# Kernel optimization log

Measured on AMD Instinct MI355X. Metric: run time of the kernel, lower is better.

Reference implementation:

```python
import jax, jax.numpy as jnp
import numpy as np
import math

NUM_HEADS = 16
MAX_BIAS = 8.0

def _alibi_slopes(n_heads):
    def slopes(n):
        start = 2.0 ** (-2 ** (-(math.log2(n) - 3)))
        return [start * start ** i for i in range(n)]
    if math.log2(n_heads).is_integer():
        s = slopes(n_heads)
    else:
        p = 2 ** math.floor(math.log2(n_heads))
        s = slopes(p) + slopes(2 * p)[0::2][: n_heads - p]
    return jnp.asarray(np.array(s, dtype=np.float32))

def setup_inputs() -> dict:
    key = jax.random.key(0)
    ks = jax.random.split(key, 5)
    B, S, C = 2, 2048, 1024
    return {
        "x": jax.random.normal(ks[0], (B, S, C), jnp.float32),
        "in_proj_weight": jax.random.normal(ks[1], (3 * C, C), jnp.float32) * (C ** -0.5),
        "in_proj_bias": jax.random.normal(ks[2], (3 * C,), jnp.float32) * 0.02,
        "out_proj_weight": jax.random.normal(ks[3], (C, C), jnp.float32) * (C ** -0.5),
        "out_proj_bias": jax.random.normal(ks[4], (C,), jnp.float32) * 0.02,
    }

def reference(x, in_proj_weight, in_proj_bias, out_proj_weight, out_proj_bias):
    B, S, C = x.shape
    H = NUM_HEADS
    D = C // H
    # fused qkv projection: [B,S,3C] -> [3,B,H,S,D]
    qkv = x @ in_proj_weight.T + in_proj_bias
    qkv = qkv.reshape(B, S, 3, H, D).transpose(2, 0, 3, 1, 4)
    q, k, v = qkv[0], qkv[1], qkv[2]
    # ALiBi bias: slopes[h] * (i - j), clamped above at MAX_BIAS -> [H,S,S]
    slopes = _alibi_slopes(H)
    pos = jnp.arange(S, dtype=jnp.float32)
    rel = pos[:, None] - pos[None, :]  # [S,S]
    bias = jnp.minimum(rel[None, :, :] * slopes[:, None, None], MAX_BIAS)
    # scores [B,H,S,S]
    scores = jnp.einsum("bhqd,bhkd->bhqk", q, k) * (D ** -0.5) + bias[None]
    probs = jax.nn.softmax(scores, axis=-1)
    out = jnp.einsum("bhqk,bhkd->bhqd", probs, v)
    out = out.transpose(0, 2, 1, 3).reshape(B, S, C)
    return out @ out_proj_weight.T + out_proj_bias
```

## Files before the change

### kernel.cpp

```cpp
#include <hip/hip_runtime.h>
#include <hip/hip_bf16.h>

typedef __bf16 bf16;
typedef __bf16 bf16x8 __attribute__((ext_vector_type(8)));
typedef __bf16 bf16x4 __attribute__((ext_vector_type(4)));
typedef float  f32x4  __attribute__((ext_vector_type(4)));

#define LOG2E 1.44269504088896340736f


__device__ __forceinline__ void gl_lds16(const void* g, void* l) {
  __builtin_amdgcn_global_load_lds((__attribute__((address_space(1))) void*)g,
                                   (__attribute__((address_space(3))) void*)l,
                                   16, 0, 0);
}

__device__ __forceinline__ unsigned cvt_pk(float lo, float hi) {
  unsigned r;
  asm("v_cvt_pk_bf16_f32 %0, %1, %2" : "=v"(r) : "v"(lo), "v"(hi));
  return r;
}

__device__ __forceinline__ bf16x8 bits8(const unsigned* w) {
  union { unsigned u[4]; bf16x8 v; } u;
  u.u[0] = w[0]; u.u[1] = w[1]; u.u[2] = w[2]; u.u[3] = w[3];
  return u.v;
}

__global__ void cvt3_kernel(const float* __restrict__ x,
                            const float* __restrict__ w1,
                            const float* __restrict__ w2,
                            bf16* __restrict__ xb,
                            bf16* __restrict__ w1b,
                            bf16* __restrict__ w2b) {
  const int NX = 1048576, NW1 = 786432, NW2 = 262144;
  const int total = NX + NW1 + NW2;
  int i = blockIdx.x * blockDim.x + threadIdx.x;
  const int stride = gridDim.x * blockDim.x;
  for (; i < total; i += stride) {
    const float* s; bf16* d; int j;
    if (i < NX)            { s = x;  d = xb;  j = i; }
    else if (i < NX + NW1) { s = w1; d = w1b; j = i - NX; }
    else                   { s = w2; d = w2b; j = i - NX - NW1; }
    f32x4 v = ((const f32x4*)s)[j];
    bf16x4 o;
    o[0] = (bf16)v[0]; o[1] = (bf16)v[1]; o[2] = (bf16)v[2]; o[3] = (bf16)v[3];
    ((bf16x4*)d)[j] = o;
  }
}

template<int EPI>
__global__ __launch_bounds__(256) void gemm_bt(const bf16* __restrict__ A,
                                               const bf16* __restrict__ Bw,
                                               const float* __restrict__ bias,
                                               void* __restrict__ outp,
                                               int M, int N, int K) {
  __shared__ bf16 As[128 * 64];
  __shared__ bf16 Bs[128 * 64];
  const int tid  = threadIdx.x;
  const int lane = tid & 63;
  const int w    = tid >> 6;
  const int wm   = w >> 1, wn = w & 1;
  const int mBase = blockIdx.y * 128;
  const int nBase = blockIdx.x * 128;
  const int rl = lane & 15;
  const int qg = lane >> 4;
  const int srow = tid >> 3;
  const int schunk = tid & 7;

  f32x4 acc[4][4] = {};

  for (int k0 = 0; k0 < K; k0 += 64) {
    __syncthreads();
#pragma unroll
    for (int rr = 0; rr < 4; ++rr) {
      int r  = rr * 32 + srow;
      int cs = schunk ^ (r & 7);
      gl_lds16(A  + (size_t)(mBase + r) * K + k0 + cs * 8, As + r * 64 + schunk * 8);
      gl_lds16(Bw + (size_t)(nBase + r) * K + k0 + cs * 8, Bs + r * 64 + schunk * 8);
    }
    __syncthreads();
#pragma unroll
    for (int ks = 0; ks < 2; ++ks) {
      bf16x8 af[4], bfr[4];
      const int cl = ks * 4 + qg;
#pragma unroll
      for (int mf = 0; mf < 4; ++mf) {
        int r = wm * 64 + mf * 16 + rl;
        af[mf] = *(const bf16x8*)(As + r * 64 + (cl ^ (r & 7)) * 8);
      }
#pragma unroll
      for (int nf = 0; nf < 4; ++nf) {
        int r = wn * 64 + nf * 16 + rl;
        bfr[nf] = *(const bf16x8*)(Bs + r * 64 + (cl ^ (r & 7)) * 8);
      }
#pragma unroll
      for (int mf = 0; mf < 4; ++mf)
#pragma unroll
        for (int nf = 0; nf < 4; ++nf)
          acc[mf][nf] = __builtin_amdgcn_mfma_f32_16x16x32_bf16(af[mf], bfr[nf],
                                                                acc[mf][nf], 0, 0, 0);
    }
  }

#pragma unroll
  for (int mf = 0; mf < 4; ++mf) {
#pragma unroll
    for (int nf = 0; nf < 4; ++nf) {
      int n = nBase + wn * 64 + nf * 16 + rl;
      float bv = bias[n];
#pragma unroll
      for (int j = 0; j < 4; ++j) {
        int m = mBase + wm * 64 + mf * 16 + qg * 4 + j;
        float val = acc[mf][nf][j] + bv;
        if (EPI == 0) {
          int t = n >> 10, rem = n & 1023;
          int h = rem >> 6, d = rem & 63;
          int b = m >> 11, s = m & 2047;
          bf16* q = (bf16*)outp;
          size_t hb = (size_t)(b * 16 + h);
          if (t == 0) {
            q[(hb * 2048 + s) * 64 + d] = (bf16)(val * (0.125f * LOG2E));
          } else if (t == 1) {
            q[4194304 + (hb * 2048 + s) * 64 + d] = (bf16)val;
          } else {
            q[8388608 + (hb * 64 + d) * 2048 + s] = (bf16)val;
          }
        } else {
          ((float*)outp)[(size_t)m * N + n] = val;
        }
      }
    }
  }
}

__global__ __launch_bounds__(256) void attn_kernel(const bf16* __restrict__ qkv,
                                                   bf16* __restrict__ attout) {
  __shared__ bf16 Ks[64 * 64];
  __shared__ bf16 Vt[64 * 64];
  __shared__ bf16 ONES[16 * 64];

  const int tid  = threadIdx.x;
  const int lane = tid & 63;
  const int w    = tid >> 6;
  const int id  = blockIdx.x;
  const int xcd = id & 7;
  const int sel = (id >> 3) & 1;
  const int b   = (id >> 4) & 1;
  const int qt  = id >> 5;
  const int h   = sel ? (15 - xcd) : xcd;
  const int bh  = b * 16 + h;
  const size_t headoff = (size_t)bh * 131072;
  const bf16* Qg = qkv + headoff;
  const bf16* Kg = qkv + 4194304 + headoff;
  const bf16* Vg = qkv + 8388608 + headoff;

  const int rl = lane & 15;
  const int qg = lane >> 4;
  const int srow = tid >> 3;
  const int schunk = tid & 7;
  const int cs8 = (schunk ^ (srow & 7)) * 8;

  ((bf16x4*)ONES)[tid] = bf16x4{(bf16)1.f, (bf16)1.f, (bf16)1.f, (bf16)1.f};

  const int qrow = qt * 64 + w * 16 + rl;
  bf16x8 qf[2];
  qf[0] = *(const bf16x8*)(Qg + (size_t)qrow * 64 + qg * 8);
  qf[1] = *(const bf16x8*)(Qg + (size_t)qrow * 64 + 32 + qg * 8);

  int koff[4][2], ooff[2];
#pragma unroll
  for (int cf = 0; cf < 4; ++cf) {
    int r = cf * 16 + rl, r7 = r & 7;
#pragma unroll
    for (int ks = 0; ks < 2; ++ks)
      koff[cf][ks] = r * 64 + (((ks * 4 + qg) ^ r7) << 3);
  }
#pragma unroll
  for (int ks = 0; ks < 2; ++ks)
    ooff[ks] = rl * 64 + (((ks * 4 + qg) ^ (rl & 7)) << 3);

  const bf16* ksrc = Kg + (size_t)srow * 64 + cs8;
  const bf16* vsrc = Vg + (size_t)srow * 2048 + cs8;
  bf16* kdst = Ks + srow * 64 + schunk * 8;
  bf16* vdst = Vt + srow * 64 + schunk * 8;

  const float slope2 = exp2f(-0.5f * (float)(h + 1)) * LOG2E;
  const float nslope = -slope2;
  const float kstep  = slope2 * 64.0f;
  float basep = slope2 * (float)(qrow - qg * 4);
  float Mm    = 8.0f * LOG2E;

  const float q0f = (float)(qt * 64);
  int ktEnd = (int)floorf((q0f + 63.f + 40.f / slope2) * (1.f / 64.f)) + 1;
  if (ktEnd > 32) ktEnd = 32;
  int ktClamp = (int)floorf((q0f - 63.f - 11.6f / slope2) * (1.f / 64.f)) + 1;
  if (ktClamp < 0) ktClamp = 0;

  f32x4 o[5] = {};

  for (int kt = 0; kt < ktEnd; ++kt) {
    __syncthreads();
    gl_lds16(ksrc,             kdst);
    gl_lds16(ksrc + 32 * 64,   kdst + 32 * 64);
    gl_lds16(vsrc,             vdst);
    gl_lds16(vsrc + 32 * 2048, vdst + 32 * 64);
    ksrc += 64 * 64; vsrc += 64;
    __syncthreads();

    f32x4 sc[4] = {};
    __builtin_amdgcn_s_setprio(1);
#pragma unroll
    for (int cf = 0; cf < 4; ++cf)
#pragma unroll
      for (int ks = 0; ks < 2; ++ks) {
        bf16x8 kf = *(const bf16x8*)(Ks + koff[cf][ks]);
        sc[cf] = __builtin_amdgcn_mfma_f32_16x16x32_bf16(kf, qf[ks], sc[cf], 0, 0, 0);
      }
    __builtin_amdgcn_s_setprio(0);

    float pe[4][4];
    if (kt >= ktClamp) {
#pragma unroll
      for (int cf = 0; cf < 4; ++cf)
#pragma unroll
        for (int j = 0; j < 4; ++j)
          pe[cf][j] = sc[cf][j] +
              fminf(__builtin_fmaf(nslope, (float)(cf * 16 + j), basep), Mm);
    } else {
#pragma unroll
      for (int cf = 0; cf < 4; ++cf)
#pragma unroll
        for (int j = 0; j < 4; ++j)
          pe[cf][j] = sc[cf][j] + Mm;
    }
    float mxa = fmaxf(fmaxf(pe[0][0], pe[0][1]), fmaxf(pe[0][2], pe[0][3]));
    float mxb = fmaxf(fmaxf(pe[1][0], pe[1][1]), fmaxf(pe[1][2], pe[1][3]));
    float mxc = fmaxf(fmaxf(pe[2][0], pe[2][1]), fmaxf(pe[2][2], pe[2][3]));
    float mxd = fmaxf(fmaxf(pe[3][0], pe[3][1]), fmaxf(pe[3][2], pe[3][3]));
    float mx = fmaxf(fmaxf(mxa, mxb), fmaxf(mxc, mxd));
    mx = fmaxf(mx, __shfl_xor(mx, 16));
    mx = fmaxf(mx, __shfl_xor(mx, 32));

    if (__any(mx > 8.0f)) {
      float d = fmaxf(mx, 0.0f);
      basep -= d; Mm -= d;
      float alpha = exp2f(-d);
      float av[4];
#pragma unroll
      for (int j = 0; j < 4; ++j)
        av[j] = __shfl(alpha, qg * 4 + j);
#pragma unroll
      for (int dg = 0; dg < 5; ++dg)
#pragma unroll
        for (int j = 0; j < 4; ++j)
          o[dg][j] *= av[j];
#pragma unroll
      for (int cf = 0; cf < 4; ++cf)
#pragma unroll
        for (int j = 0; j < 4; ++j)
          pe[cf][j] = exp2f(pe[cf][j] - d);
    } else {
#pragma unroll
      for (int cf = 0; cf < 4; ++cf)
#pragma unroll
        for (int j = 0; j < 4; ++j)
          pe[cf][j] = exp2f(pe[cf][j]);
    }

    unsigned Wd[4][2];
#pragma unroll
    for (int cf = 0; cf < 4; ++cf) {
      Wd[cf][0] = cvt_pk(pe[cf][0], pe[cf][1]);
      Wd[cf][1] = cvt_pk(pe[cf][2], pe[cf][3]);
    }
    const bool hi32  = (lane & 32) != 0;
    const bool odd16 = (lane & 16) != 0;
    unsigned Aown[2], Aoth[2], Bown[2], Both[2];
#pragma unroll
    for (int u = 0; u < 2; ++u) {
      Aown[u] = hi32 ? Wd[1][u] : Wd[0][u];
      Aoth[u] = (unsigned)__shfl_xor((int)(hi32 ? Wd[0][u] : Wd[1][u]), 32);
      Bown[u] = hi32 ? Wd[3][u] : Wd[2][u];
      Both[u] = (unsigned)__shfl_xor((int)(hi32 ? Wd[2][u] : Wd[3][u]), 32);
    }
    const bool sendOwn = odd16 ^ hi32;
    unsigned fa[4], fb[4];
#pragma unroll
    for (int u = 0; u < 2; ++u) {
      unsigned rA = (unsigned)__shfl_xor((int)(sendOwn ? Aown[u] : Aoth[u]), 16);
      unsigned rB = (unsigned)__shfl_xor((int)(sendOwn ? Bown[u] : Both[u]), 16);
      fa[u]     = odd16 ? rA : (hi32 ? Aoth[u] : Aown[u]);
      fa[2 + u] = odd16 ? (hi32 ? Aown[u] : Aoth[u]) : rA;
      fb[u]     = odd16 ? rB : (hi32 ? Both[u] : Bown[u]);
      fb[2 + u] = odd16 ? (hi32 ? Bown[u] : Both[u]) : rB;
    }
    bf16x8 pa0 = bits8(fa), pa1 = bits8(fb);

    __builtin_amdgcn_s_setprio(1);
#pragma unroll
    for (int dg = 0; dg < 4; ++dg) {
      bf16x8 vb = *(const bf16x8*)(Vt + koff[dg][0]);
      o[dg] = __builtin_amdgcn_mfma_f32_16x16x32_bf16(pa0, vb, o[dg], 0, 0, 0);
    }
    {
      bf16x8 vb = *(const bf16x8*)(ONES + ooff[0]);
      o[4] = __builtin_amdgcn_mfma_f32_16x16x32_bf16(pa0, vb, o[4], 0, 0, 0);
    }
#pragma unroll
    for (int dg = 0; dg < 4; ++dg) {
      bf16x8 vb = *(const bf16x8*)(Vt + koff[dg][1]);
      o[dg] = __builtin_amdgcn_mfma_f32_16x16x32_bf16(pa1, vb, o[dg], 0, 0, 0);
    }
    {
      bf16x8 vb = *(const bf16x8*)(ONES + ooff[1]);
      o[4] = __builtin_amdgcn_mfma_f32_16x16x32_bf16(pa1, vb, o[4], 0, 0, 0);
    }
    __builtin_amdgcn_s_setprio(0);

    basep -= kstep;
  }

  float inv[4];
#pragma unroll
  for (int j = 0; j < 4; ++j)
    inv[j] = 1.0f / o[4][j];

#pragma unroll
  for (int dg = 0; dg < 4; ++dg)
#pragma unroll
    for (int j = 0; j < 4; ++j) {
      int row = qt * 64 + w * 16 + qg * 4 + j;
      int col = h * 64 + dg * 16 + rl;
      attout[((size_t)b * 2048 + row) * 1024 + col] = (bf16)(o[dg][j] * inv[j]);
    }
}

extern "C" void kernel_launch(void* const* d_in, const int* in_sizes, int n_in,
                              void* d_out, int out_size, void* d_ws, size_t ws_size,
                              hipStream_t stream) {
  const float* x  = (const float*)d_in[0];
  const float* w1 = (const float*)d_in[1];
  const float* b1 = (const float*)d_in[2];
  const float* w2 = (const float*)d_in[3];
  const float* b2 = (const float*)d_in[4];
  float* out = (float*)d_out;

  char* ws = (char*)d_ws;
  bf16* xb    = (bf16*)(ws);
  bf16* w1b   = (bf16*)(ws + 8388608);
  bf16* w2b   = (bf16*)(ws + 14680064);
  bf16* qkvb  = (bf16*)(ws + 16777216);
  bf16* attnb = (bf16*)(ws + 41943040);

  cvt3_kernel<<<2048, 256, 0, stream>>>(x, w1, w2, xb, w1b, w2b);
  gemm_bt<0><<<dim3(24, 32), 256, 0, stream>>>(xb, w1b, b1, (void*)qkvb, 4096, 3072, 1024);
  attn_kernel<<<1024, 256, 0, stream>>>(qkvb, attnb);
  gemm_bt<1><<<dim3(8, 32), 256, 0, stream>>>(attnb, w2b, b2, (void*)out, 4096, 1024, 1024);
}
```

Measured before the change: 169.2 us.

## Double-buffer K/V tiles in attention kernel to overlap loads with compute

Doubles the LDS K and V tiles and issues the global-to-LDS async loads for the next key tile before computing the current one. The loop now ends with a vmcnt(0) wait plus a single barrier instead of two barriers around a blocking load. This aims to hide global load latency behind the MFMA and softmax work. In exchange it doubles LDS use, which may reduce occupancy.

```diff
diff --git a/kernel.cpp b/kernel.cpp
--- a/kernel.cpp
+++ b/kernel.cpp
@@ -136,8 +136,8 @@
 
 __global__ __launch_bounds__(256) void attn_kernel(const bf16* __restrict__ qkv,
                                                    bf16* __restrict__ attout) {
-  __shared__ bf16 Ks[64 * 64];
-  __shared__ bf16 Vt[64 * 64];
+  __shared__ bf16 Ks[2][64 * 64];
+  __shared__ bf16 Vt[2][64 * 64];
   __shared__ bf16 ONES[16 * 64];
 
   const int tid  = threadIdx.x;
@@ -180,10 +180,19 @@
   for (int ks = 0; ks < 2; ++ks)
     ooff[ks] = rl * 64 + (((ks * 4 + qg) ^ (rl & 7)) << 3);
 
-  const bf16* ksrc = Kg + (size_t)srow * 64 + cs8;
-  const bf16* vsrc = Vg + (size_t)srow * 2048 + cs8;
-  bf16* kdst = Ks + srow * 64 + schunk * 8;
-  bf16* vdst = Vt + srow * 64 + schunk * 8;
+#define STAGE(buf, kt_) do {                                                  \
+    const bf16* kp_ = Kg + (size_t)((kt_) * 64 + srow) * 64 + cs8;            \
+    gl_lds16(kp_,           Ks[buf] + srow * 64 + schunk * 8);                \
+    gl_lds16(kp_ + 32 * 64, Ks[buf] + (srow + 32) * 64 + schunk * 8);         \
+    const bf16* vp_ = Vg + (size_t)srow * 2048 + (kt_) * 64 + cs8;            \
+    gl_lds16(vp_,             Vt[buf] + srow * 64 + schunk * 8);              \
+    gl_lds16(vp_ + 32 * 2048, Vt[buf] + (srow + 32) * 64 + schunk * 8);       \
+  } while (0)
+
+#define DRAIN_BARRIER() do {                                                  \
+    asm volatile("s_waitcnt vmcnt(0)" ::: "memory");                          \
+    __syncthreads();                                                          \
+  } while (0)
 
   const float slope2 = exp2f(-0.5f * (float)(h + 1)) * LOG2E;
   const float nslope = -slope2;
@@ -199,14 +208,14 @@
 
   f32x4 o[5] = {};
 
+  STAGE(0, 0);
+  DRAIN_BARRIER();
+
   for (int kt = 0; kt < ktEnd; ++kt) {
-    __syncthreads();
-    gl_lds16(ksrc,             kdst);
-    gl_lds16(ksrc + 32 * 64,   kdst + 32 * 64);
-    gl_lds16(vsrc,             vdst);
-    gl_lds16(vsrc + 32 * 2048, vdst + 32 * 64);
-    ksrc += 64 * 64; vsrc += 64;
-    __syncthreads();
+    const int cur = kt & 1;
+    if (kt + 1 < ktEnd) STAGE(cur ^ 1, kt + 1);
+    const bf16* Kb = Ks[cur];
+    const bf16* Vb = Vt[cur];
 
     f32x4 sc[4] = {};
     __builtin_amdgcn_s_setprio(1);
@@ -214,7 +223,7 @@
     for (int cf = 0; cf < 4; ++cf)
 #pragma unroll
       for (int ks = 0; ks < 2; ++ks) {
-        bf16x8 kf = *(const bf16x8*)(Ks + koff[cf][ks]);
+        bf16x8 kf = *(const bf16x8*)(Kb + koff[cf][ks]);
         sc[cf] = __builtin_amdgcn_mfma_f32_16x16x32_bf16(kf, qf[ks], sc[cf], 0, 0, 0);
       }
     __builtin_amdgcn_s_setprio(0);
@@ -300,7 +309,7 @@
     __builtin_amdgcn_s_setprio(1);
 #pragma unroll
     for (int dg = 0; dg < 4; ++dg) {
-      bf16x8 vb = *(const bf16x8*)(Vt + koff[dg][0]);
+      bf16x8 vb = *(const bf16x8*)(Vb + koff[dg][0]);
       o[dg] = __builtin_amdgcn_mfma_f32_16x16x32_bf16(pa0, vb, o[dg], 0, 0, 0);
     }
     {
@@ -309,7 +318,7 @@
     }
 #pragma unroll
     for (int dg = 0; dg < 4; ++dg) {
-      bf16x8 vb = *(const bf16x8*)(Vt + koff[dg][1]);
+      bf16x8 vb = *(const bf16x8*)(Vb + koff[dg][1]);
       o[dg] = __builtin_amdgcn_mfma_f32_16x16x32_bf16(pa1, vb, o[dg], 0, 0, 0);
     }
     {
@@ -319,7 +328,11 @@
     __builtin_amdgcn_s_setprio(0);
 
     basep -= kstep;
-  }
+
+    DRAIN_BARRIER();
+  }
+#undef STAGE
+#undef DRAIN_BARRIER
 
   float inv[4];
 #pragma unroll
```

Result: slower. 174.3 us (+3.0%).

## Halve attention block to 32 query rows, reverse tile order, drop LDS ones tile

Applied to the files above, without the earlier changes.

The attention kernel now uses 128-thread blocks, each covering 32 query rows, so the grid doubles to 2048 blocks. Query tiles are launched in reverse order so the long-running late tiles start first. Each block still loads the full 64x64 K/V tile, now with 4 loads per thread. The ones tile held in LDS for the row-sum MFMA is replaced by a register constant. The intent is better load balance and more resident blocks, at the cost of twice the K/V tile traffic per query row.

```diff
diff --git a/kernel.cpp b/kernel.cpp
--- a/kernel.cpp
+++ b/kernel.cpp
@@ -134,22 +134,21 @@
   }
 }
 
-__global__ __launch_bounds__(256) void attn_kernel(const bf16* __restrict__ qkv,
+__global__ __launch_bounds__(128) void attn_kernel(const bf16* __restrict__ qkv,
                                                    bf16* __restrict__ attout) {
   __shared__ bf16 Ks[64 * 64];
   __shared__ bf16 Vt[64 * 64];
-  __shared__ bf16 ONES[16 * 64];
 
   const int tid  = threadIdx.x;
   const int lane = tid & 63;
   const int w    = tid >> 6;
-  const int id  = blockIdx.x;
-  const int xcd = id & 7;
-  const int sel = (id >> 3) & 1;
-  const int b   = (id >> 4) & 1;
-  const int qt  = id >> 5;
-  const int h   = sel ? (15 - xcd) : xcd;
-  const int bh  = b * 16 + h;
+  const int id   = blockIdx.x;
+  const int xcd  = id & 7;
+  const int sel  = (id >> 3) & 1;
+  const int b    = (id >> 4) & 1;
+  const int qt   = 63 - (id >> 5);
+  const int h    = sel ? (15 - xcd) : xcd;
+  const int bh   = b * 16 + h;
   const size_t headoff = (size_t)bh * 131072;
   const bf16* Qg = qkv + headoff;
   const bf16* Kg = qkv + 4194304 + headoff;
@@ -157,18 +156,20 @@
 
   const int rl = lane & 15;
   const int qg = lane >> 4;
-  const int srow = tid >> 3;
+  const int srow0  = tid >> 3;
   const int schunk = tid & 7;
-  const int cs8 = (schunk ^ (srow & 7)) * 8;
-
-  ((bf16x4*)ONES)[tid] = bf16x4{(bf16)1.f, (bf16)1.f, (bf16)1.f, (bf16)1.f};
-
-  const int qrow = qt * 64 + w * 16 + rl;
+  const int cs8 = (schunk ^ (srow0 & 7)) * 8;
+
+  const int qrow = qt * 32 + w * 16 + rl;
   bf16x8 qf[2];
   qf[0] = *(const bf16x8*)(Qg + (size_t)qrow * 64 + qg * 8);
   qf[1] = *(const bf16x8*)(Qg + (size_t)qrow * 64 + 32 + qg * 8);
 
-  int koff[4][2], ooff[2];
+  bf16x8 vones;
+#pragma unroll
+  for (int e = 0; e < 8; ++e) vones[e] = (bf16)1.0f;
+
+  int koff[4][2];
 #pragma unroll
   for (int cf = 0; cf < 4; ++cf) {
     int r = cf * 16 + rl, r7 = r & 7;
@@ -176,14 +177,11 @@
     for (int ks = 0; ks < 2; ++ks)
       koff[cf][ks] = r * 64 + (((ks * 4 + qg) ^ r7) << 3);
   }
-#pragma unroll
-  for (int ks = 0; ks < 2; ++ks)
-    ooff[ks] = rl * 64 + (((ks * 4 + qg) ^ (rl & 7)) << 3);
-
-  const bf16* ksrc = Kg + (size_t)srow * 64 + cs8;
-  const bf16* vsrc = Vg + (size_t)srow * 2048 + cs8;
-  bf16* kdst = Ks + srow * 64 + schunk * 8;
-  bf16* vdst = Vt + srow * 64 + schunk * 8;
+
+  const bf16* ksrc = Kg + (size_t)srow0 * 64 + cs8;
+  const bf16* vsrc = Vg + (size_t)srow0 * 2048 + cs8;
+  bf16* kdst = Ks + srow0 * 64 + schunk * 8;
+  bf16* vdst = Vt + srow0 * 64 + schunk * 8;
 
   const float slope2 = exp2f(-0.5f * (float)(h + 1)) * LOG2E;
   const float nslope = -slope2;
@@ -191,8 +189,8 @@
   float basep = slope2 * (float)(qrow - qg * 4);
   float Mm    = 8.0f * LOG2E;
 
-  const float q0f = (float)(qt * 64);
-  int ktEnd = (int)floorf((q0f + 63.f + 40.f / slope2) * (1.f / 64.f)) + 1;
+  const float q0f = (float)(qt * 32);
+  int ktEnd = (int)floorf((q0f + 31.f + 40.f / slope2) * (1.f / 64.f)) + 1;
   if (ktEnd > 32) ktEnd = 32;
   int ktClamp = (int)floorf((q0f - 63.f - 11.6f / slope2) * (1.f / 64.f)) + 1;
   if (ktClamp < 0) ktClamp = 0;
@@ -201,10 +199,12 @@
 
   for (int kt = 0; kt < ktEnd; ++kt) {
     __syncthreads();
-    gl_lds16(ksrc,             kdst);
-    gl_lds16(ksrc + 32 * 64,   kdst + 32 * 64);
-    gl_lds16(vsrc,             vdst);
-    gl_lds16(vsrc + 32 * 2048, vdst + 32 * 64);
+#pragma unroll
+    for (int i = 0; i < 4; ++i)
+      gl_lds16(ksrc + i * 16 * 64, kdst + i * 16 * 64);
+#pragma unroll
+    for (int i = 0; i < 4; ++i)
+      gl_lds16(vsrc + (size_t)i * 16 * 2048, vdst + i * 16 * 64);
     ksrc += 64 * 64; vsrc += 64;
     __syncthreads();
 
@@ -303,19 +303,13 @@
       bf16x8 vb = *(const bf16x8*)(Vt + koff[dg][0]);
       o[dg] = __builtin_amdgcn_mfma_f32_16x16x32_bf16(pa0, vb, o[dg], 0, 0, 0);
     }
-    {
-      bf16x8 vb = *(const bf16x8*)(ONES + ooff[0]);
-      o[4] = __builtin_amdgcn_mfma_f32_16x16x32_bf16(pa0, vb, o[4], 0, 0, 0);
-    }
+    o[4] = __builtin_amdgcn_mfma_f32_16x16x32_bf16(pa0, vones, o[4], 0, 0, 0);
 #pragma unroll
     for (int dg = 0; dg < 4; ++dg) {
       bf16x8 vb = *(const bf16x8*)(Vt + koff[dg][1]);
       o[dg] = __builtin_amdgcn_mfma_f32_16x16x32_bf16(pa1, vb, o[dg], 0, 0, 0);
     }
-    {
-      bf16x8 vb = *(const bf16x8*)(ONES + ooff[1]);
-      o[4] = __builtin_amdgcn_mfma_f32_16x16x32_bf16(pa1, vb, o[4], 0, 0, 0);
-    }
+    o[4] = __builtin_amdgcn_mfma_f32_16x16x32_bf16(pa1, vones, o[4], 0, 0, 0);
     __builtin_amdgcn_s_setprio(0);
 
     basep -= kstep;
@@ -330,7 +324,7 @@
   for (int dg = 0; dg < 4; ++dg)
 #pragma unroll
     for (int j = 0; j < 4; ++j) {
-      int row = qt * 64 + w * 16 + qg * 4 + j;
+      int row = qt * 32 + w * 16 + qg * 4 + j;
       int col = h * 64 + dg * 16 + rl;
       attout[((size_t)b * 2048 + row) * 1024 + col] = (bf16)(o[dg][j] * inv[j]);
     }
@@ -355,6 +349,6 @@
 
   cvt3_kernel<<<2048, 256, 0, stream>>>(x, w1, w2, xb, w1b, w2b);
   gemm_bt<0><<<dim3(24, 32), 256, 0, stream>>>(xb, w1b, b1, (void*)qkvb, 4096, 3072, 1024);
-  attn_kernel<<<1024, 256, 0, stream>>>(qkvb, attnb);
+  attn_kernel<<<2048, 128, 0, stream>>>(qkvb, attnb);
   gemm_bt<1><<<dim3(8, 32), 256, 0, stream>>>(attnb, w2b, b2, (void*)out, 4096, 1024, 1024);
 }
```

Result: slower. 190.0 us (+12.2%).
